# Performance work log

Measured on AMD Instinct MI355X. Metric: run time of the kernel, lower is better.

## Reference

```python
import jax, jax.numpy as jnp
import numpy as np

NUM_HEADS = 16
ROPE_THETA = 10000.0


def apply_rope(x, pos):
    # x: [b, h, s, d_head]; rotates consecutive pairs (2i, 2i+1)
    d = x.shape[-1]
    inv_freq = ROPE_THETA ** (-jnp.arange(0, d, 2, dtype=x.dtype) / d)  # [d/2]
    ang = pos.astype(x.dtype)[:, None] * inv_freq[None, :]              # [s, d/2]
    cos, sin = jnp.cos(ang), jnp.sin(ang)
    x1, x2 = x[..., 0::2], x[..., 1::2]
    rot = jnp.stack([x1 * cos - x2 * sin, x1 * sin + x2 * cos], axis=-1)
    return rot.reshape(x.shape)


def setup_inputs() -> dict:
    key = jax.random.key(0)
    k1, k2, k3 = jax.random.split(key, 3)
    d_model = 1024
    x = jax.random.normal(k1, (4, 2048, d_model), dtype=jnp.float32)
    wqkv = jax.random.normal(k2, (3 * d_model, d_model), dtype=jnp.float32) * 0.02
    wout = jax.random.normal(k3, (d_model, d_model), dtype=jnp.float32) * 0.02
    return {"x": x, "wqkv": wqkv, "wout": wout}


def reference(x, wqkv, wout):
    b, s, d_model = x.shape
    h = NUM_HEADS
    d_head = d_model // h

    qkv = jnp.einsum("bsd,ed->bse", x, wqkv)              # [b, s, 3*d_model]
    q, k, v = jnp.split(qkv, 3, axis=-1)

    def split_heads(t):  # [b, s, d_model] -> [b, h, s, d_head]
        return t.reshape(b, s, h, d_head).transpose(0, 2, 1, 3)

    q, k, v = split_heads(q), split_heads(k), split_heads(v)

    pos = jnp.arange(s)
    q = apply_rope(q, pos)
    k = apply_rope(k, pos)

    scale = 1.0 / jnp.sqrt(jnp.asarray(d_head, dtype=x.dtype))
    scores = jnp.einsum("bhqd,bhkd->bhqk", q, k) * scale   # [b, h, s, s]
    causal = jnp.tril(jnp.ones((s, s), dtype=bool))
    scores = jnp.where(causal, scores, jnp.finfo(scores.dtype).min)
    attn = jax.nn.softmax(scores, axis=-1)
    y = jnp.einsum("bhqk,bhkd->bhqd", attn, v)             # [b, h, s, d_head]
    y = y.transpose(0, 2, 1, 3).reshape(b, s, d_model)
    return jnp.einsum("bsd,ed->bse", y, wout)
```

## Files before the change

kernel.cpp:

```cpp
#include <hip/hip_runtime.h>
#include <stdint.h>

typedef uint16_t u16;
typedef __bf16 bf16x8 __attribute__((ext_vector_type(8)));
typedef float   f32x4 __attribute__((ext_vector_type(4)));
typedef uint16_t u16x2 __attribute__((ext_vector_type(2)));
typedef uint16_t u16x4 __attribute__((ext_vector_type(4)));
typedef uint16_t u16x8 __attribute__((ext_vector_type(8)));
typedef float   f32x4g __attribute__((ext_vector_type(4)));

#define DEV __device__ __forceinline__

DEV u16 f2bf(float f) {
  __bf16 h = (__bf16)f;
  return __builtin_bit_cast(u16, h);
}
DEV float bf2f(u16 u) {
  union { uint32_t u; float f; } v; v.u = ((uint32_t)u) << 16;
  return v.f;
}
DEV float exp2fast(float x) {
  float r; asm("v_exp_f32 %0, %1" : "=v"(r) : "v"(x)); return r;
}

DEV void gload_lds16(const u16* g, u16* l) {
  __builtin_amdgcn_global_load_lds((const __attribute__((address_space(1))) void*)g,
                                   (__attribute__((address_space(3))) void*)l,
                                   16, 0, 0);
}

__global__ void cvt3_kernel(const float* __restrict__ a, u16* __restrict__ da,
                            const float* __restrict__ b, u16* __restrict__ db,
                            const float* __restrict__ c, u16* __restrict__ dc) {
  int i = blockIdx.x * 256 + threadIdx.x;
  const float* s; u16* d; int off;
  if (i < 2097152)      { s = a; d = da; off = i; }
  else if (i < 2883584) { s = b; d = db; off = i - 2097152; }
  else                  { s = c; d = dc; off = i - 2883584; }
  f32x4g v = ((const f32x4g*)s)[off];
  u16 tmp[4] = {f2bf(v[0]), f2bf(v[1]), f2bf(v[2]), f2bf(v[3])};
  *(uint64_t*)(d + (size_t)off * 4) = *(const uint64_t*)tmp;
}

template<bool OUT_BF16>
__global__ __launch_bounds__(256) void gemm_bt(const u16* __restrict__ A,
                                               const u16* __restrict__ B,
                                               void* __restrict__ Cv,
                                               int M, int N, int K) {
  constexpr int BK = 32;
  __shared__ __align__(16) u16 As[2][128 * BK];
  __shared__ __align__(16) u16 Bs[2][128 * BK];
  const int t = threadIdx.x;
  const int w = t >> 6, l = t & 63;
  const int l4 = l >> 4, l15 = l & 15;

  const int nbx = gridDim.x;
  const int nwg = gridDim.x * gridDim.y;
  const int orig = blockIdx.y * nbx + blockIdx.x;
  const int wgid = (orig & 7) * (nwg >> 3) + (orig >> 3);
  const int bm = (wgid / nbx) * 128, bn = (wgid % nbx) * 128;

  const int wr = (w >> 1) * 64, wc = (w & 1) * 64;

  const int srow = w * 32 + (l >> 2);
  const int scol = (l & 3) * 8;
  const u16* gA = A + (size_t)(bm + srow) * K + scol;
  const u16* gB = B + (size_t)(bn + srow) * K + scol;

  f32x4 acc[4][4];
#pragma unroll
  for (int m = 0; m < 4; ++m)
#pragma unroll
    for (int n = 0; n < 4; ++n) acc[m][n] = f32x4{0.f, 0.f, 0.f, 0.f};

  const int nkt = K / BK;

  auto stage = [&](int kt, int buf) {
    const u16* a0 = gA + (size_t)kt * BK;
    const u16* b0 = gB + (size_t)kt * BK;
    gload_lds16(a0,                  &As[buf][(w * 32) * BK]);
    gload_lds16(a0 + (size_t)16 * K, &As[buf][(w * 32 + 16) * BK]);
    gload_lds16(b0,                  &Bs[buf][(w * 32) * BK]);
    gload_lds16(b0 + (size_t)16 * K, &Bs[buf][(w * 32 + 16) * BK]);
  };

  stage(0, 0);
  __syncthreads();
  for (int kt = 0; kt < nkt; ++kt) {
    const int buf = kt & 1;
    if (kt + 1 < nkt) stage(kt + 1, buf ^ 1);
    bf16x8 af[4], bfr[4];
#pragma unroll
    for (int m = 0; m < 4; ++m) af[m]  = *(const bf16x8*)&As[buf][(wr + m * 16 + l15) * BK + l4 * 8];
#pragma unroll
    for (int n = 0; n < 4; ++n) bfr[n] = *(const bf16x8*)&Bs[buf][(wc + n * 16 + l15) * BK + l4 * 8];
#pragma unroll
    for (int m = 0; m < 4; ++m)
#pragma unroll
      for (int n = 0; n < 4; ++n)
        acc[m][n] = __builtin_amdgcn_mfma_f32_16x16x32_bf16(af[m], bfr[n], acc[m][n], 0, 0, 0);
    __syncthreads();
  }

#pragma unroll
  for (int m = 0; m < 4; ++m) {
    const int row0 = bm + wr + m * 16 + l4 * 4;
#pragma unroll
    for (int n = 0; n < 4; ++n) {
      const int col = bn + wc + n * 16 + l15;
#pragma unroll
      for (int r = 0; r < 4; ++r) {
        if (OUT_BF16) ((u16*)Cv)[(size_t)(row0 + r) * N + col] = f2bf(acc[m][n][r]);
        else          ((float*)Cv)[(size_t)(row0 + r) * N + col] = acc[m][n][r];
      }
    }
  }
}

__global__ void rope_kernel(const u16* __restrict__ qkv, u16* __restrict__ Qh, u16* __restrict__ Kh) {
  const int idx = blockIdx.x * 256 + threadIdx.x;
  const int i = idx & 31;
  const int h = (idx >> 5) & 15;
  const int s = (idx >> 9) & 2047;
  const int b = idx >> 20;
  const size_t row = (size_t)b * 2048 + s;
  const u16* q = qkv + row * 3072 + h * 64 + 2 * i;
  const float invf = (float)exp2(-2.0 * (double)i / 64.0 * 13.287712379549449);
  const float ang = (float)s * invf;
  float sn, cs;
  sincosf(ang, &sn, &cs);
  const size_t orow = ((size_t)(b * 16 + h) * 2048 + s) * 64 + 2 * i;
  constexpr float QS = 0.125f * 1.4426950408889634f;
  {
    u16x2 qp = *(const u16x2*)q;
    float x1 = bf2f(qp[0]), x2 = bf2f(qp[1]);
    u16x2 o; o[0] = f2bf((x1 * cs - x2 * sn) * QS); o[1] = f2bf((x1 * sn + x2 * cs) * QS);
    *(u16x2*)(Qh + orow) = o;
  }
  {
    u16x2 kp = *(const u16x2*)(q + 1024);
    float x1 = bf2f(kp[0]), x2 = bf2f(kp[1]);
    u16x2 o; o[0] = f2bf(x1 * cs - x2 * sn); o[1] = f2bf(x1 * sn + x2 * cs);
    *(u16x2*)(Kh + orow) = o;
  }
}

__global__ __launch_bounds__(256) void vtrans_kernel(const u16* __restrict__ qkv, u16* __restrict__ Vt) {
  __shared__ u16 Ls[64][68];
  const int t = threadIdx.x;
  const int st = blockIdx.x;
  const int bh = blockIdx.y;
  const int b = bh >> 4, h = bh & 15;
  const int s0 = st * 64;
#pragma unroll
  for (int c = t; c < 512; c += 256) {
    const int sr = c >> 3, ch = c & 7;
    u16x8 v = *(const u16x8*)(qkv + ((size_t)b * 2048 + s0 + sr) * 3072 + 2048 + h * 64 + ch * 8);
#pragma unroll
    for (int j = 0; j < 8; ++j) Ls[sr][ch * 8 + j] = v[j];
  }
  __syncthreads();
#pragma unroll
  for (int c = t; c < 512; c += 256) {
    const int d = c >> 3, sch = c & 7;
    u16x8 o;
#pragma unroll
    for (int j = 0; j < 8; ++j) o[j] = Ls[sch * 8 + j][d];
    *(u16x8*)(Vt + ((size_t)bh * 64 + d) * 2048 + s0 + sch * 8) = o;
  }
}

__global__ __launch_bounds__(256) void attn_kernel(const u16* __restrict__ Qh,
                                                   const u16* __restrict__ Kh,
                                                   const u16* __restrict__ Vt,
                                                   u16* __restrict__ Y) {
  __shared__ __align__(16) u16 Ks[64][72];
  __shared__ __align__(16) u16 Vs[64][72];
  __shared__ __align__(16) u16 Ps[4][32][72];
  const int t = threadIdx.x, w = t >> 6, l = t & 63;
  const int l4 = l >> 4, l15 = l & 15;
  const int bid = blockIdx.x;
  const int p   = (bid >> 3) & 15;
  const int bh  = ((bid >> 7) << 3) | (bid & 7);
  const int b = bh >> 4, h = bh & 15;
  const int qb0 = p * 64 + w * 16;
  const int qb1 = (31 - p) * 64 + w * 16;
  const u16* Qb = Qh + (size_t)bh * 2048 * 64;
  const u16* Kb = Kh + (size_t)bh * 2048 * 64;
  const u16* Vb = Vt + (size_t)bh * 64 * 2048;

  bf16x8 qf[2][2];
  {
    const int qb[2] = {qb0, qb1};
#pragma unroll
    for (int m = 0; m < 2; ++m)
#pragma unroll
      for (int ks = 0; ks < 2; ++ks)
        qf[m][ks] = *(const bf16x8*)(Qb + (size_t)(qb[m] + l15) * 64 + ks * 32 + l4 * 8);
  }

  f32x4 o[2][4];
#pragma unroll
  for (int m = 0; m < 2; ++m)
#pragma unroll
    for (int nd = 0; nd < 4; ++nd) o[m][nd] = f32x4{0.f, 0.f, 0.f, 0.f};
  float lsum[2] = {0.f, 0.f};

  const int sr = t >> 3;
  const int scol = (t & 7) * 8;
  const int nkv = 32 - p;

  u16x8 rk0 = *(const u16x8*)(Kb + (size_t)sr * 64 + scol);
  u16x8 rk1 = *(const u16x8*)(Kb + (size_t)(sr + 32) * 64 + scol);
  u16x8 rv0 = *(const u16x8*)(Vb + (size_t)sr * 2048 + scol);
  u16x8 rv1 = *(const u16x8*)(Vb + (size_t)(sr + 32) * 2048 + scol);

  for (int kv = 0; kv < nkv; ++kv) {
    const int kv0 = kv * 64;
    __syncthreads();
    *(u16x8*)&Ks[sr][scol]      = rk0;
    *(u16x8*)&Ks[sr + 32][scol] = rk1;
    *(u16x8*)&Vs[sr][scol]      = rv0;
    *(u16x8*)&Vs[sr + 32][scol] = rv1;
    __syncthreads();
    if (kv + 1 < nkv) {
      const int n0 = kv0 + 64;
      rk0 = *(const u16x8*)(Kb + (size_t)(n0 + sr) * 64 + scol);
      rk1 = *(const u16x8*)(Kb + (size_t)(n0 + sr + 32) * 64 + scol);
      rv0 = *(const u16x8*)(Vb + (size_t)sr * 2048 + n0 + scol);
      rv1 = *(const u16x8*)(Vb + (size_t)(sr + 32) * 2048 + n0 + scol);
    }

    auto SCORE = [&](int m, int qbm) {
      f32x4 sfr[4];
      __builtin_amdgcn_s_setprio(1);
#pragma unroll
      for (int n = 0; n < 4; ++n) {
        bf16x8 kf0 = *(const bf16x8*)&Ks[n * 16 + l15][l4 * 8];
        bf16x8 kf1 = *(const bf16x8*)&Ks[n * 16 + l15][32 + l4 * 8];
        f32x4 a = f32x4{0.f, 0.f, 0.f, 0.f};
        a = __builtin_amdgcn_mfma_f32_16x16x32_bf16(kf0, qf[m][0], a, 0, 0, 0);
        a = __builtin_amdgcn_mfma_f32_16x16x32_bf16(kf1, qf[m][1], a, 0, 0, 0);
        sfr[n] = a;
      }
      __builtin_amdgcn_s_setprio(0);
      if (kv0 + 63 > qbm) {
        const int q = qbm + l15;
#pragma unroll
        for (int n = 0; n < 4; ++n)
#pragma unroll
          for (int r = 0; r < 4; ++r)
            if (kv0 + n * 16 + l4 * 4 + r > q) sfr[n][r] = -1e30f;
      }
      float rs = 0.f;
#pragma unroll
      for (int n = 0; n < 4; ++n) {
#pragma unroll
        for (int r = 0; r < 4; ++r) {
          const float pv = exp2fast(sfr[n][r]);
          sfr[n][r] = pv; rs += pv;
        }
        u16x4 pk = {f2bf(sfr[n][0]), f2bf(sfr[n][1]), f2bf(sfr[n][2]), f2bf(sfr[n][3])};
        *(u16x4*)&Ps[w][m * 16 + l15][n * 16 + l4 * 4] = pk;
      }
      lsum[m] += rs;
    };

    SCORE(1, qb1);
    if (kv <= p) SCORE(0, qb0);

    bf16x8 vfr[4][2];
#pragma unroll
    for (int nd = 0; nd < 4; ++nd) {
      vfr[nd][0] = *(const bf16x8*)&Vs[nd * 16 + l15][l4 * 8];
      vfr[nd][1] = *(const bf16x8*)&Vs[nd * 16 + l15][32 + l4 * 8];
    }

    auto PV = [&](int m) {
      bf16x8 pf0 = *(const bf16x8*)&Ps[w][m * 16 + l15][l4 * 8];
      bf16x8 pf1 = *(const bf16x8*)&Ps[w][m * 16 + l15][32 + l4 * 8];
      __builtin_amdgcn_s_setprio(1);
#pragma unroll
      for (int nd = 0; nd < 4; ++nd) {
        o[m][nd] = __builtin_amdgcn_mfma_f32_16x16x32_bf16(pf0, vfr[nd][0], o[m][nd], 0, 0, 0);
        o[m][nd] = __builtin_amdgcn_mfma_f32_16x16x32_bf16(pf1, vfr[nd][1], o[m][nd], 0, 0, 0);
      }
      __builtin_amdgcn_s_setprio(0);
    };
    PV(1);
    if (kv <= p) PV(0);
  }

  const int qb[2] = {qb0, qb1};
#pragma unroll
  for (int m = 0; m < 2; ++m) {
    lsum[m] += __shfl_xor(lsum[m], 16);
    lsum[m] += __shfl_xor(lsum[m], 32);
    const float li = 1.0f / lsum[m];
    float lb[4];
#pragma unroll
    for (int r = 0; r < 4; ++r) lb[r] = __shfl(li, (l & 48) | (l4 * 4 + r));
#pragma unroll
    for (int r = 0; r < 4; ++r) {
      const size_t row = (size_t)b * 2048 + qb[m] + l4 * 4 + r;
#pragma unroll
      for (int nd = 0; nd < 4; ++nd)
        Y[row * 1024 + h * 64 + nd * 16 + l15] = f2bf(o[m][nd][r] * lb[r]);
    }
  }
}

extern "C" void kernel_launch(void* const* d_in, const int* in_sizes, int n_in,
                              void* d_out, int out_size, void* d_ws, size_t ws_size,
                              hipStream_t stream) {
  const float* x    = (const float*)d_in[0];
  const float* wqkv = (const float*)d_in[1];
  const float* wout = (const float*)d_in[2];
  float* out = (float*)d_out;
  char* ws = (char*)d_ws;

  u16* x_bf    = (u16*)(ws);
  u16* Y       = x_bf;
  u16* wqkv_bf = (u16*)(ws + 16777216);
  u16* wout_bf = (u16*)(ws + 23068672);
  u16* qkv_bf  = (u16*)(ws + 25165824);
  u16* Qh      = (u16*)(ws + 75497472);
  u16* Kh      = (u16*)(ws + 92274688);
  u16* Vt      = (u16*)(ws + 109051904);

  cvt3_kernel<<<12288, 256, 0, stream>>>(x, x_bf, wqkv, wqkv_bf, wout, wout_bf);
  gemm_bt<true><<<dim3(24, 64), 256, 0, stream>>>(x_bf, wqkv_bf, qkv_bf, 8192, 3072, 1024);
  rope_kernel<<<16384, 256, 0, stream>>>(qkv_bf, Qh, Kh);
  vtrans_kernel<<<dim3(32, 64), 256, 0, stream>>>(qkv_bf, Vt);
  attn_kernel<<<1024, 256, 0, stream>>>(Qh, Kh, Vt, Y);
  gemm_bt<false><<<dim3(8, 64), 256, 0, stream>>>(Y, wout_bf, out, 8192, 1024, 1024);
}
```

Measured before the change: 207.4 us.

## Fuse RoPE, Q scaling and V transpose into QKV GEMM epilogue

Replaces the generic QKV GEMM plus separate rope and V-transpose kernels with a single GEMM whose epilogue writes Q/K in head-major layout with RoPE applied (using a precomputed sin/cos table and lane shuffles for pair partners) and writes V directly transposed. This removes the write and re-read of the intermediate qkv buffer and two kernel launches. In exchange the epilogue does scattered 2-byte stores with per-element table loads, and a small table kernel is added.

```diff
diff --git a/kernel.cpp b/kernel.cpp
--- a/kernel.cpp
+++ b/kernel.cpp
@@ -27,6 +27,15 @@
   __builtin_amdgcn_global_load_lds((const __attribute__((address_space(1))) void*)g,
                                    (__attribute__((address_space(3))) void*)l,
                                    16, 0, 0);
+}
+
+__global__ void sctab_kernel(float2* __restrict__ tab) {
+  const int idx = blockIdx.x * 256 + threadIdx.x;
+  const int s = idx >> 5, i = idx & 31;
+  const float invf = (float)exp2(-2.0 * (double)i / 64.0 * 13.287712379549449);
+  float sn, cs;
+  sincosf((float)s * invf, &sn, &cs);
+  tab[idx] = make_float2(cs, sn);
 }
 
 __global__ void cvt3_kernel(const float* __restrict__ a, u16* __restrict__ da,
@@ -42,6 +51,109 @@
   *(uint64_t*)(d + (size_t)off * 4) = *(const uint64_t*)tmp;
 }
 
+__global__ __launch_bounds__(256) void gemm_qkv(const u16* __restrict__ A,
+                                                const u16* __restrict__ B,
+                                                const float2* __restrict__ tab,
+                                                u16* __restrict__ Qh,
+                                                u16* __restrict__ Kh,
+                                                u16* __restrict__ Vt) {
+  constexpr int K = 1024;
+  constexpr int BK = 32;
+  __shared__ __align__(16) u16 As[2][128 * BK];
+  __shared__ __align__(16) u16 Bs[2][128 * BK];
+  const int t = threadIdx.x;
+  const int w = t >> 6, l = t & 63;
+  const int l4 = l >> 4, l15 = l & 15;
+
+  const int nbx = gridDim.x;
+  const int nwg = gridDim.x * gridDim.y;
+  const int orig = blockIdx.y * nbx + blockIdx.x;
+  const int wgid = (orig & 7) * (nwg >> 3) + (orig >> 3);
+  const int bm = (wgid / nbx) * 128, bn = (wgid % nbx) * 128;
+
+  const int wr = (w >> 1) * 64, wc = (w & 1) * 64;
+
+  const int srow = w * 32 + (l >> 2);
+  const int scol = (l & 3) * 8;
+  const u16* gA = A + (size_t)(bm + srow) * K + scol;
+  const u16* gB = B + (size_t)(bn + srow) * K + scol;
+
+  f32x4 acc[4][4];
+#pragma unroll
+  for (int m = 0; m < 4; ++m)
+#pragma unroll
+    for (int n = 0; n < 4; ++n) acc[m][n] = f32x4{0.f, 0.f, 0.f, 0.f};
+
+  const int nkt = K / BK;
+
+  auto stage = [&](int kt, int buf) {
+    const u16* a0 = gA + (size_t)kt * BK;
+    const u16* b0 = gB + (size_t)kt * BK;
+    gload_lds16(a0,                  &As[buf][(w * 32) * BK]);
+    gload_lds16(a0 + (size_t)16 * K, &As[buf][(w * 32 + 16) * BK]);
+    gload_lds16(b0,                  &Bs[buf][(w * 32) * BK]);
+    gload_lds16(b0 + (size_t)16 * K, &Bs[buf][(w * 32 + 16) * BK]);
+  };
+
+  stage(0, 0);
+  __syncthreads();
+  for (int kt = 0; kt < nkt; ++kt) {
+    const int buf = kt & 1;
+    if (kt + 1 < nkt) stage(kt + 1, buf ^ 1);
+    bf16x8 af[4], bfr[4];
+#pragma unroll
+    for (int m = 0; m < 4; ++m) af[m]  = *(const bf16x8*)&As[buf][(wr + m * 16 + l15) * BK + l4 * 8];
+#pragma unroll
+    for (int n = 0; n < 4; ++n) bfr[n] = *(const bf16x8*)&Bs[buf][(wc + n * 16 + l15) * BK + l4 * 8];
+#pragma unroll
+    for (int m = 0; m < 4; ++m)
+#pragma unroll
+      for (int n = 0; n < 4; ++n)
+        acc[m][n] = __builtin_amdgcn_mfma_f32_16x16x32_bf16(af[m], bfr[n], acc[m][n], 0, 0, 0);
+    __syncthreads();
+  }
+
+  const int part = bn >> 10;
+  const int ccbase = (bn & 1023) + wc;
+  if (part == 2) {
+#pragma unroll
+    for (int m = 0; m < 4; ++m) {
+      const int row0 = bm + wr + m * 16 + l4 * 4;
+      const int bb = row0 >> 11, s0 = row0 & 2047;
+#pragma unroll
+      for (int n = 0; n < 4; ++n) {
+        const int cc = ccbase + n * 16 + l15;
+        const int hh = cc >> 6, dd = cc & 63;
+        u16x4 pk = {f2bf(acc[m][n][0]), f2bf(acc[m][n][1]), f2bf(acc[m][n][2]), f2bf(acc[m][n][3])};
+        *(u16x4*)(Vt + ((size_t)(bb * 16 + hh) * 64 + dd) * 2048 + s0) = pk;
+      }
+    }
+  } else {
+    const float qs = (part == 0) ? 0.18033688011112042f : 1.0f;
+    u16* const Out = (part == 0) ? Qh : Kh;
+#pragma unroll
+    for (int m = 0; m < 4; ++m) {
+      const int row0 = bm + wr + m * 16 + l4 * 4;
+      const int bb = row0 >> 11, s0 = row0 & 2047;
+#pragma unroll
+      for (int n = 0; n < 4; ++n) {
+        const int cc = ccbase + n * 16 + l15;
+        const int hh = cc >> 6, dd = cc & 63;
+        const int fi = dd >> 1;
+        const float sgn = (dd & 1) ? 1.f : -1.f;
+        u16* outp = Out + ((size_t)(bb * 16 + hh) * 2048 + s0) * 64 + dd;
+#pragma unroll
+        for (int r = 0; r < 4; ++r) {
+          const float a = acc[m][n][r];
+          const float other = __shfl_xor(a, 1);
+          const float2 cs2 = tab[(size_t)(s0 + r) * 32 + fi];
+          outp[(size_t)r * 64] = f2bf((a * cs2.x + other * sgn * cs2.y) * qs);
+        }
+      }
+    }
+  }
+}
+
 template<bool OUT_BF16>
 __global__ __launch_bounds__(256) void gemm_bt(const u16* __restrict__ A,
                                                const u16* __restrict__ B,
@@ -114,59 +226,6 @@
         else          ((float*)Cv)[(size_t)(row0 + r) * N + col] = acc[m][n][r];
       }
     }
-  }
-}
-
-__global__ void rope_kernel(const u16* __restrict__ qkv, u16* __restrict__ Qh, u16* __restrict__ Kh) {
-  const int idx = blockIdx.x * 256 + threadIdx.x;
-  const int i = idx & 31;
-  const int h = (idx >> 5) & 15;
-  const int s = (idx >> 9) & 2047;
-  const int b = idx >> 20;
-  const size_t row = (size_t)b * 2048 + s;
-  const u16* q = qkv + row * 3072 + h * 64 + 2 * i;
-  const float invf = (float)exp2(-2.0 * (double)i / 64.0 * 13.287712379549449);
-  const float ang = (float)s * invf;
-  float sn, cs;
-  sincosf(ang, &sn, &cs);
-  const size_t orow = ((size_t)(b * 16 + h) * 2048 + s) * 64 + 2 * i;
-  constexpr float QS = 0.125f * 1.4426950408889634f;
-  {
-    u16x2 qp = *(const u16x2*)q;
-    float x1 = bf2f(qp[0]), x2 = bf2f(qp[1]);
-    u16x2 o; o[0] = f2bf((x1 * cs - x2 * sn) * QS); o[1] = f2bf((x1 * sn + x2 * cs) * QS);
-    *(u16x2*)(Qh + orow) = o;
-  }
-  {
-    u16x2 kp = *(const u16x2*)(q + 1024);
-    float x1 = bf2f(kp[0]), x2 = bf2f(kp[1]);
-    u16x2 o; o[0] = f2bf(x1 * cs - x2 * sn); o[1] = f2bf(x1 * sn + x2 * cs);
-    *(u16x2*)(Kh + orow) = o;
-  }
-}
-
-__global__ __launch_bounds__(256) void vtrans_kernel(const u16* __restrict__ qkv, u16* __restrict__ Vt) {
-  __shared__ u16 Ls[64][68];
-  const int t = threadIdx.x;
-  const int st = blockIdx.x;
-  const int bh = blockIdx.y;
-  const int b = bh >> 4, h = bh & 15;
-  const int s0 = st * 64;
-#pragma unroll
-  for (int c = t; c < 512; c += 256) {
-    const int sr = c >> 3, ch = c & 7;
-    u16x8 v = *(const u16x8*)(qkv + ((size_t)b * 2048 + s0 + sr) * 3072 + 2048 + h * 64 + ch * 8);
-#pragma unroll
-    for (int j = 0; j < 8; ++j) Ls[sr][ch * 8 + j] = v[j];
-  }
-  __syncthreads();
-#pragma unroll
-  for (int c = t; c < 512; c += 256) {
-    const int d = c >> 3, sch = c & 7;
-    u16x8 o;
-#pragma unroll
-    for (int j = 0; j < 8; ++j) o[j] = Ls[sch * 8 + j][d];
-    *(u16x8*)(Vt + ((size_t)bh * 64 + d) * 2048 + s0 + sch * 8) = o;
   }
 }
 
@@ -323,15 +382,14 @@
   u16* Y       = x_bf;
   u16* wqkv_bf = (u16*)(ws + 16777216);
   u16* wout_bf = (u16*)(ws + 23068672);
-  u16* qkv_bf  = (u16*)(ws + 25165824);
+  float2* tab  = (float2*)(ws + 25165824);
   u16* Qh      = (u16*)(ws + 75497472);
   u16* Kh      = (u16*)(ws + 92274688);
   u16* Vt      = (u16*)(ws + 109051904);
 
+  sctab_kernel<<<256, 256, 0, stream>>>(tab);
   cvt3_kernel<<<12288, 256, 0, stream>>>(x, x_bf, wqkv, wqkv_bf, wout, wout_bf);
-  gemm_bt<true><<<dim3(24, 64), 256, 0, stream>>>(x_bf, wqkv_bf, qkv_bf, 8192, 3072, 1024);
-  rope_kernel<<<16384, 256, 0, stream>>>(qkv_bf, Qh, Kh);
-  vtrans_kernel<<<dim3(32, 64), 256, 0, stream>>>(qkv_bf, Vt);
+  gemm_qkv<<<dim3(24, 64), 256, 0, stream>>>(x_bf, wqkv_bf, tab, Qh, Kh, Vt);
   attn_kernel<<<1024, 256, 0, stream>>>(Qh, Kh, Vt, Y);
   gemm_bt<false><<<dim3(8, 64), 256, 0, stream>>>(Y, wout_bf, out, 8192, 1024, 1024);
 }
```

Result: no change. 204.4 us (-1.5%).
